# Kernel optimization log

Measured on AMD Instinct MI355X. Metric: run time of the kernel, lower is better.

The kernel has to match this reference:

```python
import jax, jax.numpy as jnp
import numpy as np

B, CIN, H, W = 32, 512, 16, 16
COUT, HEADS, SPARSITY = 2048, 8, 7
D = COUT // HEADS  # 256, must equal H*W
N = H * W


def conv1x1(x, w, b):
    # x: [B,C,H,W], w: [O,C], b: [O]
    return jnp.einsum('bchw,oc->bohw', x, w) + b[None, :, None, None]


def setup_inputs() -> dict:
    key = jax.random.key(0)
    ks = jax.random.split(key, 11)
    def lin(k, o, c):
        bound = 1.0 / np.sqrt(c)
        kw, kb = jax.random.split(k)
        return (jax.random.uniform(kw, (o, c), jnp.float32, -bound, bound),
                jax.random.uniform(kb, (o,), jnp.float32, -bound, bound))
    Wq, bq = lin(ks[0], COUT, CIN)
    Wk, bk = lin(ks[1], COUT, CIN)
    Wv, bv = lin(ks[2], COUT, CIN)
    Wo, bo = lin(ks[3], COUT, COUT)
    # kaiming_uniform_ on [COUT, COUT]
    gain = np.sqrt(2.0) / np.sqrt(5.0)  # default a=sqrt(5)
    bound = gain * np.sqrt(3.0 / COUT)
    coeff = jax.random.uniform(ks[4], (COUT, COUT), jnp.float32, -bound, bound)
    scale = jnp.array([np.sqrt(D)], jnp.float32)
    x = jax.random.normal(ks[5], (B, CIN, H, W), jnp.float32)
    return {"x": x, "Wq": Wq, "bq": bq, "Wk": Wk, "bk": bk, "Wv": Wv,
            "bv": bv, "Wo": Wo, "bo": bo, "coeff": coeff, "scale": scale}


def reference(x, Wq, bq, Wk, bk, Wv, bv, Wo, bo, coeff, scale):
    # enforce_sparsity: keep top-`SPARSITY` |coeff| per row, zero the rest
    _, idx = jax.lax.top_k(jnp.abs(coeff), SPARSITY)  # [COUT, SPARSITY]
    mask = jnp.zeros(coeff.shape, bool).at[jnp.arange(COUT)[:, None], idx].set(True)
    coeff_s = jnp.where(mask, coeff, 0.0)

    q = conv1x1(x, Wq, bq).reshape(B, HEADS, D, N)
    k = conv1x1(x, Wk, bk).reshape(B, HEADS, D, N)
    v = conv1x1(x, Wv, bv).reshape(B, HEADS, D, N)

    attn = jnp.einsum('bhdn,bhdm->bhnm', q, k) / scale[0]  # [B,h,N,N]
    sparse_attn = jnp.einsum('bhnm,mp->bhnp', attn, coeff_s[:D, :D])
    sparse_attn = jax.nn.softmax(sparse_attn, axis=-1)
    out = jnp.einsum('bhnm,bhmd->bhnd', sparse_attn, v.transpose(0, 1, 3, 2))
    out = out.transpose(0, 1, 3, 2).reshape(B, COUT, H, W)
    return conv1x1(out, Wo, bo)
```

## Files before the change

kernel.cpp:

```cpp
#include <hip/hip_runtime.h>

typedef unsigned short ushort;
typedef __attribute__((ext_vector_type(8))) short short8;
typedef __attribute__((ext_vector_type(8))) unsigned short ushort8;
typedef __attribute__((ext_vector_type(4))) unsigned short ushort4v;
typedef __attribute__((ext_vector_type(4))) float fx4;

#define MAXNNZ (256*7)

__device__ __forceinline__ ushort f2bf(float f) {
    union { float f; unsigned u; } v; v.f = f;
    unsigned r = v.u + 0x7fffu + ((v.u >> 16) & 1u);
    return (ushort)(r >> 16);
}

__device__ __forceinline__ float bf2f(ushort b) {
    union { unsigned u; float f; } v; v.u = ((unsigned)b) << 16;
    return v.f;
}

__device__ __forceinline__ void gload_lds16(const ushort* g, ushort* l) {
    __builtin_amdgcn_global_load_lds(
        (const __attribute__((address_space(1))) unsigned int*)g,
        (__attribute__((address_space(3))) unsigned int*)l, 16, 0, 0);
}

__global__ __launch_bounds__(256)
void topk_kernel(const float* __restrict__ coeff,
                 int* __restrict__ coo_cnt, int* __restrict__ coo_m,
                 int* __restrict__ coo_p, float* __restrict__ coo_v)
{
    int row = blockIdx.x;
    int tid = threadIdx.x;
    const float* crow = coeff + (long)row * 2048;
    float av[8];
#pragma unroll
    for (int i = 0; i < 8; ++i) av[i] = fabsf(crow[tid + 256 * i]);
    __shared__ unsigned long long red[256];
    for (int t = 0; t < 7; ++t) {
        float mx = -1.f; int mi = 0;
#pragma unroll
        for (int i = 0; i < 8; ++i) if (av[i] > mx) { mx = av[i]; mi = i; }
        unsigned col = (unsigned)(tid + 256 * mi);
        unsigned long long pk = ((unsigned long long)__float_as_uint(mx) << 32)
                              | (unsigned long long)(2048u - col);
        red[tid] = pk; __syncthreads();
        for (int s = 128; s > 0; s >>= 1) {
            if (tid < s) { if (red[tid + s] > red[tid]) red[tid] = red[tid + s]; }
            __syncthreads();
        }
        unsigned long long w = red[0];
        __syncthreads();
        unsigned wcol = 2048u - (unsigned)(w & 0xffffffffu);
        if ((wcol & 255u) == (unsigned)tid) av[wcol >> 8] = -1.f;
        if (tid == 0 && wcol < 256u) {
            int pos = atomicAdd(coo_cnt, 1);
            coo_m[pos] = row; coo_p[pos] = (int)wcol; coo_v[pos] = crow[wcol];
        }
    }
}

__global__ __launch_bounds__(256)
void csc_kernel(const int* __restrict__ coo_cnt, const int* __restrict__ coo_m,
                const int* __restrict__ coo_p, const float* __restrict__ coo_v,
                int* __restrict__ csc_ptr, int* __restrict__ csc_m, float* __restrict__ csc_v)
{
    __shared__ int cnt[256];
    __shared__ int off[257];
    __shared__ int cur[256];
    int tid = threadIdx.x;
    cnt[tid] = 0;
    __syncthreads();
    int n = *coo_cnt; if (n > MAXNNZ) n = MAXNNZ;
    for (int e = tid; e < n; e += 256) atomicAdd(&cnt[coo_p[e]], 1);
    __syncthreads();
    if (tid == 0) {
        int s = 0;
        for (int p = 0; p < 256; ++p) { off[p] = s; s += cnt[p]; }
        off[256] = s;
    }
    __syncthreads();
    csc_ptr[tid] = off[tid];
    if (tid == 0) csc_ptr[256] = off[256];
    cur[tid] = off[tid];
    __syncthreads();
    for (int e = tid; e < n; e += 256) {
        int p = coo_p[e];
        int pos = atomicAdd(&cur[p], 1);
        csc_m[pos] = coo_m[e];
        csc_v[pos] = coo_v[e];
    }
}

__global__ void cvt4_kernel(const float* a0, ushort* d0, int n0,
                            const float* a1, ushort* d1, int n1,
                            const float* a2, ushort* d2, int n2,
                            const float* a3, ushort* d3, int n3)
{
    const float* s; ushort* d; int n;
    switch (blockIdx.y) {
        case 0: s = a0; d = d0; n = n0; break;
        case 1: s = a1; d = d1; n = n1; break;
        case 2: s = a2; d = d2; n = n2; break;
        default: s = a3; d = d3; n = n3; break;
    }
    int nv = n >> 2;
    for (int i = blockIdx.x * blockDim.x + threadIdx.x; i < nv; i += gridDim.x * blockDim.x) {
        fx4 v = ((const fx4*)s)[i];
        ushort4v o;
        o[0] = f2bf(v[0]); o[1] = f2bf(v[1]); o[2] = f2bf(v[2]); o[3] = f2bf(v[3]);
        ((ushort4v*)d)[i] = o;
    }
}

__global__ __launch_bounds__(256)
void transpose_f32_bf16(const float* __restrict__ in, ushort* __restrict__ out, int R, int C)
{
    int z = blockIdx.z;
    const float* ib = in + (long)z * R * C;
    ushort* ob = out + (long)z * R * C;
    __shared__ ushort tile[64][72];
    int r0 = blockIdx.x * 64, c0 = blockIdx.y * 64;
    int tid = threadIdx.x;
    int rl = tid >> 2, sg = tid & 3;
#pragma unroll
    for (int h = 0; h < 4; ++h) {
        fx4 v = *(const fx4*)(ib + (long)(r0 + rl) * C + c0 + h * 16 + sg * 4);
#pragma unroll
        for (int i = 0; i < 4; ++i) tile[h * 16 + sg * 4 + i][rl] = f2bf(v[i]);
    }
    __syncthreads();
    int cl = rl;
#pragma unroll
    for (int h = 0; h < 2; ++h) {
        ushort8 vv = *(const ushort8*)(&tile[cl][h * 32 + sg * 8]);
        *(ushort8*)(ob + (long)(c0 + cl) * R + r0 + h * 32 + sg * 8) = vv;
    }
}

__global__ __launch_bounds__(256)
void kcomb_kernel(const ushort* __restrict__ kbT, ushort* __restrict__ ktc,
                  const int* __restrict__ csc_ptr, const int* __restrict__ csc_m,
                  const float* __restrict__ csc_v)
{
    int z = blockIdx.y;
    int tid = threadIdx.x;
    int p = blockIdx.x * 64 + (tid >> 2);
    int d0 = (tid & 3) * 64;
    const ushort* src = kbT + (long)z * 65536;
    float acc[64];
#pragma unroll
    for (int i = 0; i < 64; ++i) acc[i] = 0.f;
    int e0 = csc_ptr[p], e1 = csc_ptr[p + 1];
    for (int e = e0; e < e1; ++e) {
        const ushort* row = src + csc_m[e] * 256 + d0;
        float c = csc_v[e];
#pragma unroll
        for (int u = 0; u < 8; ++u) {
            ushort8 v = *(const ushort8*)(row + u * 8);
#pragma unroll
            for (int t = 0; t < 8; ++t) acc[u * 8 + t] += bf2f(v[t]) * c;
        }
    }
    ushort* dst = ktc + (long)z * 65536 + (long)p * 256 + d0;
#pragma unroll
    for (int u = 0; u < 8; ++u) {
        ushort8 o;
#pragma unroll
        for (int t = 0; t < 8; ++t) o[t] = f2bf(acc[u * 8 + t]);
        *(ushort8*)(dst + u * 8) = o;
    }
}

__global__ __launch_bounds__(512)
void attn_kernel(const ushort* __restrict__ Q, const ushort* __restrict__ Kt,
                 const ushort* __restrict__ V, ushort* __restrict__ O,
                 const float* __restrict__ scale_src)
{
    int z = blockIdx.x;
    int b = z >> 3, h = z & 7;
    const ushort* Qz = Q + (long)z * 65536;
    const ushort* Kz = Kt + (long)z * 65536;
    const ushort* Vz = V + (long)b * 524288 + (long)h * 65536;
    ushort* Ob = O + (long)b * 524288 + (long)h * 256;

    __shared__ __align__(16) ushort P[128 * 256];
    __shared__ __align__(16) ushort As[128 * 32];
    __shared__ __align__(16) ushort Bs[256 * 32];
    __shared__ __align__(16) ushort Vst[2][256 * 32];
    __shared__ float rmax[4][128];
    __shared__ float rsum[4][128];

    int tid = threadIdx.x;
    int wave = tid >> 6, lane = tid & 63;
    int l16 = lane & 15, quad = lane >> 4;

    int skey = (tid >> 3) & 3;
    int scol = ((tid & 3) ^ skey) * 8;
    int srow = tid >> 2;
    const ushort* qsrc  = Qz + (long)srow * 256 + scol;
    const ushort* ksrc0 = Kz + (long)srow * 256 + scol;
    const ushort* ksrc1 = ksrc0 + 128 * 256;
    const ushort* vsrc0 = Vz + (long)srow * 256 + scol;
    const ushort* vsrc1 = vsrc0 + 128 * 256;
    ushort* aDst  = As + wave * 512;
    ushort* bDst0 = Bs + wave * 512;
    ushort* bDst1 = Bs + 4096 + wave * 512;

    int rk = (l16 >> 1) & 3;
    float sc = 1.0f / scale_src[0];

    for (int hf = 0; hf < 2; ++hf) {
        int wrow = wave >> 2, wcol = wave & 3;
        fx4 acc[4][4];
#pragma unroll
        for (int i = 0; i < 4; ++i)
#pragma unroll
            for (int j = 0; j < 4; ++j) acc[i][j] = (fx4){0.f, 0.f, 0.f, 0.f};

        const ushort* qs = qsrc + (long)hf * 128 * 256;
        for (int kc = 0; kc < 256; kc += 32) {
            __syncthreads();
            gload_lds16(qs + kc, aDst);
            gload_lds16(ksrc0 + kc, bDst0);
            gload_lds16(ksrc1 + kc, bDst1);
            __syncthreads();
            short8 af[4], bf[4];
#pragma unroll
            for (int i = 0; i < 4; ++i)
                af[i] = *(const short8*)(As + (wrow * 64 + i * 16 + l16) * 32 + ((quad ^ rk) * 8));
#pragma unroll
            for (int j = 0; j < 4; ++j)
                bf[j] = *(const short8*)(Bs + (wcol * 64 + j * 16 + l16) * 32 + ((quad ^ rk) * 8));
#pragma unroll
            for (int i = 0; i < 4; ++i)
#pragma unroll
                for (int j = 0; j < 4; ++j)
                    acc[i][j] = __builtin_amdgcn_mfma_f32_16x16x32_bf16(af[i], bf[j], acc[i][j], 0, 0, 0);
        }

#pragma unroll
        for (int i = 0; i < 4; ++i)
#pragma unroll
            for (int j = 0; j < 4; ++j)
#pragma unroll
                for (int r = 0; r < 4; ++r) acc[i][j][r] *= sc;

        float lm[4][4];
#pragma unroll
        for (int i = 0; i < 4; ++i)
#pragma unroll
            for (int r = 0; r < 4; ++r) {
                float m = -1e30f;
#pragma unroll
                for (int j = 0; j < 4; ++j) m = fmaxf(m, acc[i][j][r]);
                lm[i][r] = m;
            }
#pragma unroll
        for (int d = 1; d < 16; d <<= 1)
#pragma unroll
            for (int i = 0; i < 4; ++i)
#pragma unroll
                for (int r = 0; r < 4; ++r) lm[i][r] = fmaxf(lm[i][r], __shfl_xor(lm[i][r], d, 16));
        if (l16 == 0) {
#pragma unroll
            for (int i = 0; i < 4; ++i)
#pragma unroll
                for (int r = 0; r < 4; ++r)
                    rmax[wcol][wrow * 64 + i * 16 + quad * 4 + r] = lm[i][r];
        }
        __syncthreads();

        float ls[4][4];
#pragma unroll
        for (int i = 0; i < 4; ++i)
#pragma unroll
            for (int r = 0; r < 4; ++r) {
                int row = wrow * 64 + i * 16 + quad * 4 + r;
                float M = fmaxf(fmaxf(rmax[0][row], rmax[1][row]),
                                fmaxf(rmax[2][row], rmax[3][row]));
                float s = 0.f;
#pragma unroll
                for (int j = 0; j < 4; ++j) {
                    float e = __expf(acc[i][j][r] - M);
                    acc[i][j][r] = e;
                    s += e;
                }
                ls[i][r] = s;
            }
#pragma unroll
        for (int d = 1; d < 16; d <<= 1)
#pragma unroll
            for (int i = 0; i < 4; ++i)
#pragma unroll
                for (int r = 0; r < 4; ++r) ls[i][r] += __shfl_xor(ls[i][r], d, 16);
        if (l16 == 0) {
#pragma unroll
            for (int i = 0; i < 4; ++i)
#pragma unroll
                for (int r = 0; r < 4; ++r)
                    rsum[wcol][wrow * 64 + i * 16 + quad * 4 + r] = ls[i][r];
        }
        __syncthreads();

#pragma unroll
        for (int i = 0; i < 4; ++i)
#pragma unroll
            for (int r = 0; r < 4; ++r) {
                int row = wrow * 64 + i * 16 + quad * 4 + r;
                float inv = 1.0f / (rsum[0][row] + rsum[1][row] + rsum[2][row] + rsum[3][row]);
                int key = row & 7;
#pragma unroll
                for (int j = 0; j < 4; ++j) {
                    int p = wcol * 64 + j * 16 + l16;
                    int idx = row * 256 + ((((p >> 3) ^ key) << 3) | (p & 7));
                    P[idx] = f2bf(acc[i][j][r] * inv);
                }
            }
        __syncthreads();

        int r2 = wave >> 2, c2 = wave & 3;
        fx4 acc2[4][4];
#pragma unroll
        for (int i = 0; i < 4; ++i)
#pragma unroll
            for (int j = 0; j < 4; ++j) acc2[i][j] = (fx4){0.f, 0.f, 0.f, 0.f};

        gload_lds16(vsrc0, Vst[0] + wave * 512);
        gload_lds16(vsrc1, Vst[0] + 4096 + wave * 512);
        __syncthreads();

        for (int kk = 0; kk < 8; ++kk) {
            short8 pa[4], vf[4];
#pragma unroll
            for (int i = 0; i < 4; ++i) {
                int row = r2 * 64 + i * 16 + l16;
                pa[i] = *(const short8*)(P + row * 256 + (((kk * 4 + quad) ^ (l16 & 7)) * 8));
            }
#pragma unroll
            for (int j = 0; j < 4; ++j)
                vf[j] = *(const short8*)(Vst[kk & 1] + (c2 * 64 + j * 16 + l16) * 32 + ((quad ^ rk) * 8));
            if (kk < 7) {
                gload_lds16(vsrc0 + (kk + 1) * 32, Vst[(kk + 1) & 1] + wave * 512);
                gload_lds16(vsrc1 + (kk + 1) * 32, Vst[(kk + 1) & 1] + 4096 + wave * 512);
            }
#pragma unroll
            for (int i = 0; i < 4; ++i)
#pragma unroll
                for (int j = 0; j < 4; ++j)
                    acc2[i][j] = __builtin_amdgcn_mfma_f32_16x16x32_bf16(pa[i], vf[j], acc2[i][j], 0, 0, 0);
            __syncthreads();
        }

#pragma unroll
        for (int i = 0; i < 4; ++i)
#pragma unroll
            for (int j = 0; j < 4; ++j) {
                int rowb = r2 * 64 + i * 16 + quad * 4;
                int col = c2 * 64 + j * 16 + l16;
#pragma unroll
                for (int rr = 0; rr < 4; ++rr) {
                    int row = rowb + rr;
                    int idx = row * 256 + ((((col >> 3) ^ (row & 7)) << 3) | (col & 7));
                    P[idx] = f2bf(acc2[i][j][rr]);
                }
            }
        __syncthreads();
#pragma unroll
        for (int pass = 0; pass < 8; ++pass) {
            int row = pass * 16 + (tid >> 5), ch = tid & 31;
            ushort8 v = *(const ushort8*)(P + row * 256 + ((ch ^ (row & 7)) << 3));
            *(ushort8*)(Ob + (long)(hf * 128 + row) * 2048 + ch * 8) = v;
        }
        __syncthreads();
    }
}

template<int MODE>
__global__ __launch_bounds__(512, 2)
void gemm256(const ushort* __restrict__ A, const ushort* __restrict__ B,
             void* __restrict__ C,
             const float* __restrict__ bias0, const float* __restrict__ bias1,
             const float* __restrict__ bias2,
             int MT, int K)
{
    __shared__ __align__(16) ushort lds[4][2][8192];

    int nwg = gridDim.x;
    int bid = blockIdx.x;
    int cpx = nwg >> 3;
    int swz = (bid & 7) * cpx + (bid >> 3);
    int mt = swz % MT, nt = swz / MT;
    int m0 = mt << 8, n0 = nt << 8;

    int tid = threadIdx.x;
    int wave = tid >> 6, lane = tid & 63;
    int wr = wave >> 2, wc = wave & 3;
    int l16 = lane & 15, quad = lane >> 4;

    int lc = (((lane & 3) ^ ((lane >> 3) & 3))) * 8;
    const ushort* gA0 = A + (long long)(m0 + wave * 16 + (lane >> 2)) * K + lc;
    const ushort* gA1 = gA0 + (long long)128 * K;
    const ushort* gB0 = B + (long long)(n0 + wave * 16 + (lane >> 2)) * K + lc;
    const ushort* gB1 = gB0 + (long long)128 * K;
    int ldso = wave * 512;

    int rsw = ((l16 >> 1) & 3) * 8;
    int aoff = (wr * 128 + l16) * 32 + ((quad * 8) ^ rsw);
    int boff = (wc * 64 + l16) * 32 + ((quad * 8) ^ rsw);

    fx4 acc[8][4];
#pragma unroll
    for (int i = 0; i < 8; ++i)
#pragma unroll
        for (int j = 0; j < 4; ++j) acc[i][j] = (fx4){0.f, 0.f, 0.f, 0.f};

    auto stageA = [&](int b, int kc) {
        gload_lds16(gA0 + kc, &lds[b][0][ldso]);
        gload_lds16(gA1 + kc, &lds[b][0][4096 + ldso]);
    };
    auto stageB = [&](int b, int kc) {
        gload_lds16(gB0 + kc, &lds[b][1][ldso]);
        gload_lds16(gB1 + kc, &lds[b][1][4096 + ldso]);
    };

    short8 af[4], bf[4];
    auto readA = [&](int b, int half) {
        const ushort* p = &lds[b][0][aoff + half * 2048];
#pragma unroll
        for (int i = 0; i < 4; ++i) af[i] = *(const short8*)(p + i * 512);
    };
    auto readB = [&](int b) {
        const ushort* p = &lds[b][1][boff];
#pragma unroll
        for (int j = 0; j < 4; ++j) bf[j] = *(const short8*)(p + j * 512);
    };
    auto mma = [&](int half) {
        __builtin_amdgcn_s_setprio(1);
#pragma unroll
        for (int i = 0; i < 4; ++i)
#pragma unroll
            for (int j = 0; j < 4; ++j)
                acc[half * 4 + i][j] =
                    __builtin_amdgcn_mfma_f32_16x16x32_bf16(af[i], bf[j], acc[half * 4 + i][j], 0, 0, 0);
        __builtin_amdgcn_s_setprio(0);
    };

    int NT = K >> 5;
    stageA(0, 0);  stageB(0, 0);
    stageA(1, 32); stageB(1, 32);
    stageA(2, 64); stageB(2, 64);
    asm volatile("s_waitcnt vmcnt(8)" ::: "memory");
    __builtin_amdgcn_s_barrier();

    for (int t = 0; t < NT; ++t) {
        int b = t & 3;
        readA(b, 0); readB(b);
        if (t + 3 < NT) stageA((t + 3) & 3, (t + 3) << 5);
        __builtin_amdgcn_s_barrier();
        asm volatile("s_waitcnt lgkmcnt(0)" ::: "memory");
        __builtin_amdgcn_sched_barrier(0);
        mma(0);
        __builtin_amdgcn_s_barrier();
        readA(b, 1);
        if (t + 3 < NT) {
            stageB((t + 3) & 3, (t + 3) << 5);
            asm volatile("s_waitcnt vmcnt(8)" ::: "memory");
        } else if (t + 2 < NT) {
            asm volatile("s_waitcnt vmcnt(4)" ::: "memory");
        } else if (t + 1 < NT) {
            asm volatile("s_waitcnt vmcnt(0)" ::: "memory");
        }
        __builtin_amdgcn_s_barrier();
        asm volatile("s_waitcnt lgkmcnt(0)" ::: "memory");
        __builtin_amdgcn_sched_barrier(0);
        mma(1);
        __builtin_amdgcn_s_barrier();
    }

    if (MODE == 5) {
        float* Cf = (float*)C + (long long)nt * 524288;
#pragma unroll
        for (int i = 0; i < 8; ++i) {
            int m = m0 + wr * 128 + i * 16 + quad * 4;
#pragma unroll
            for (int j = 0; j < 4; ++j) {
                int n = wc * 64 + j * 16 + l16;
                float* dst = Cf + (long long)m * 256 + n;
#pragma unroll
                for (int r = 0; r < 4; ++r)
                    dst[(long)r * 256] = acc[i][j][r] + bias0[m + r];
            }
        }
        return;
    }

    if (MODE == 4) {
        int sec = m0 >> 11;
        int ms0 = m0 & 2047;
        ushort* ct = &lds[0][0][0];
        if (sec < 2) {
            const float* bs = (sec == 0) ? bias0 : bias1;
            ushort* base = (ushort*)C + (long long)sec * 16777216
                         + (long long)nt * 524288 + (long long)(ms0 >> 8) * 65536;
#pragma unroll
            for (int hh = 0; hh < 2; ++hh) {
                if ((wc >> 1) == hh) {
#pragma unroll
                    for (int i = 0; i < 8; ++i)
#pragma unroll
                        for (int j = 0; j < 4; ++j) {
                            int nl = (wc & 1) * 64 + j * 16 + l16;
                            int ml = wr * 128 + i * 16 + quad * 4;
                            ushort4v pk;
#pragma unroll
                            for (int r = 0; r < 4; ++r)
                                pk[r] = f2bf(acc[i][j][r] + bs[ms0 + ml + r]);
                            *(ushort4v*)(ct + nl * 264 + ml) = pk;
                        }
                }
                __syncthreads();
                int row = tid & 127, c0 = (tid >> 7) * 64;
                ushort* dst = base + (long long)(hh * 128 + row) * 256 + c0;
                const ushort* src = ct + row * 264 + c0;
#pragma unroll
                for (int u = 0; u < 8; ++u)
                    *(ushort8*)(dst + u * 8) = *(const ushort8*)(src + u * 8);
                __syncthreads();
            }
        } else {
            ushort* base = (ushort*)C + 33554432LL + (long long)nt * 524288
                         + (long long)ms0 * 256;
#pragma unroll
            for (int hh = 0; hh < 2; ++hh) {
                if (wr == hh) {
#pragma unroll
                    for (int i = 0; i < 8; ++i)
#pragma unroll
                        for (int j = 0; j < 4; ++j) {
                            int nl = wc * 64 + j * 16 + l16;
                            int ml = i * 16 + quad * 4;
#pragma unroll
                            for (int r = 0; r < 4; ++r)
                                ct[(ml + r) * 264 + nl] =
                                    f2bf(acc[i][j][r] + bias2[ms0 + hh * 128 + ml + r]);
                        }
                }
                __syncthreads();
                int row = tid & 127, c0 = (tid >> 7) * 64;
                ushort* dst = base + (long long)(hh * 128 + row) * 256 + c0;
                const ushort* src = ct + row * 264 + c0;
#pragma unroll
                for (int u = 0; u < 8; ++u)
                    *(ushort8*)(dst + u * 8) = *(const ushort8*)(src + u * 8);
                __syncthreads();
            }
        }
        return;
    }
}

extern "C" void kernel_launch(void* const* d_in, const int* in_sizes, int n_in,
                              void* d_out, int out_size, void* d_ws, size_t ws_size,
                              hipStream_t stream)
{
    const float* x     = (const float*)d_in[0];
    const float* Wq    = (const float*)d_in[1];
    const float* bq    = (const float*)d_in[2];
    const float* Wk    = (const float*)d_in[3];
    const float* bk    = (const float*)d_in[4];
    const float* Wv    = (const float*)d_in[5];
    const float* bv    = (const float*)d_in[6];
    const float* Wo    = (const float*)d_in[7];
    const float* bo    = (const float*)d_in[8];
    const float* coeff = (const float*)d_in[9];
    const float* scale = (const float*)d_in[10];
    float* out = (float*)d_out;

    size_t o = 0;
    char* w = (char*)d_ws;
    auto take = [&](size_t bytes) -> void* {
        void* p = w + o; o += (bytes + 255) & ~(size_t)255; return p;
    };
    int*    coo_cnt = (int*)take(4);
    int*    coo_m   = (int*)take(MAXNNZ * 4);
    int*    coo_p   = (int*)take(MAXNNZ * 4);
    float*  coo_v   = (float*)take(MAXNNZ * 4);
    int*    csc_ptr = (int*)take(257 * 4);
    int*    csc_m   = (int*)take(MAXNNZ * 4);
    float*  csc_v   = (float*)take(MAXNNZ * 4);
    ushort* wqkv = (ushort*)take(6144L * 512 * 2);
    ushort* wob  = (ushort*)take(2048L * 2048 * 2);
    ushort* xT   = (ushort*)take(32L * 256 * 512 * 2);
    ushort* qkv  = (ushort*)take(3 * 16777216L * 2);
    ushort* qbT = qkv;
    ushort* kbT = qkv + 16777216L;
    ushort* vb  = qkv + 33554432L;
    ushort* ktc = (ushort*)take(16777216L * 2);
    ushort* obT  = kbT;
    (void)in_sizes; (void)n_in; (void)out_size; (void)ws_size;

    hipMemsetAsync(coo_cnt, 0, 4, stream);
    topk_kernel<<<256, 256, 0, stream>>>(coeff, coo_cnt, coo_m, coo_p, coo_v);
    csc_kernel<<<1, 256, 0, stream>>>(coo_cnt, coo_m, coo_p, coo_v, csc_ptr, csc_m, csc_v);

    cvt4_kernel<<<dim3(1024, 4, 1), 256, 0, stream>>>(
        Wq, wqkv, 2048 * 512, Wk, wqkv + 2048L * 512, 2048 * 512,
        Wv, wqkv + 4096L * 512, 2048 * 512, Wo, wob, 2048 * 2048);
    transpose_f32_bf16<<<dim3(8, 4, 32), 256, 0, stream>>>(x, xT, 512, 256);

    gemm256<4><<<dim3(768, 1, 1), dim3(512, 1, 1), 0, stream>>>(
        wqkv, xT, qkv, bq, bk, bv, 24, 512);

    kcomb_kernel<<<dim3(4, 256), 256, 0, stream>>>(kbT, ktc, csc_ptr, csc_m, csc_v);

    attn_kernel<<<256, 512, 0, stream>>>(qbT, ktc, vb, obT, scale);

    gemm256<5><<<dim3(256, 1, 1), dim3(512, 1, 1), 0, stream>>>(
        wob, obT, out, bo, nullptr, nullptr, 8, 2048);
}
```

Before: 401.5 us.

## Stage full Q tile in LDS and double-buffer 64-wide K/V chunks in attention

The attention kernel now loads the whole 128x256 Q half-tile into LDS once, reusing that buffer for P, and streams K and V in 64-column chunks through a double buffer. The next chunk's load is issued before the MFMAs on the current one, and V prefetch starts during softmax normalisation. Barriers become raw s_barrier with explicit waitcnt, plus setprio around the MFMA blocks. Together these aim to cut the barrier count and expose fewer global-load stalls, at the cost of more LDS, register pressure and fragile manual synchronisation.

```diff
diff --git a/kernel.cpp b/kernel.cpp
--- a/kernel.cpp
+++ b/kernel.cpp
@@ -177,6 +177,11 @@
                  const ushort* __restrict__ V, ushort* __restrict__ O,
                  const float* __restrict__ scale_src)
 {
+    __shared__ __align__(16) ushort PQ[32768];
+    __shared__ __align__(16) ushort KV[2][16384];
+    __shared__ float rmax[4][128];
+    __shared__ float rsum[4][128];
+
     int z = blockIdx.x;
     int b = z >> 3, h = z & 7;
     const ushort* Qz = Q + (long)z * 65536;
@@ -184,59 +189,67 @@
     const ushort* Vz = V + (long)b * 524288 + (long)h * 65536;
     ushort* Ob = O + (long)b * 524288 + (long)h * 256;
 
-    __shared__ __align__(16) ushort P[128 * 256];
-    __shared__ __align__(16) ushort As[128 * 32];
-    __shared__ __align__(16) ushort Bs[256 * 32];
-    __shared__ __align__(16) ushort Vst[2][256 * 32];
-    __shared__ float rmax[4][128];
-    __shared__ float rsum[4][128];
-
     int tid = threadIdx.x;
     int wave = tid >> 6, lane = tid & 63;
     int l16 = lane & 15, quad = lane >> 4;
-
-    int skey = (tid >> 3) & 3;
-    int scol = ((tid & 3) ^ skey) * 8;
-    int srow = tid >> 2;
-    const ushort* qsrc  = Qz + (long)srow * 256 + scol;
-    const ushort* ksrc0 = Kz + (long)srow * 256 + scol;
-    const ushort* ksrc1 = ksrc0 + 128 * 256;
-    const ushort* vsrc0 = Vz + (long)srow * 256 + scol;
-    const ushort* vsrc1 = vsrc0 + 128 * 256;
-    ushort* aDst  = As + wave * 512;
-    ushort* bDst0 = Bs + wave * 512;
-    ushort* bDst1 = Bs + 4096 + wave * 512;
-
-    int rk = (l16 >> 1) & 3;
+    int wrow = wave >> 2, wcol = wave & 3;
+    int key = l16 & 7;
+
+    const ushort* ksrc = Kz + (long)(tid >> 3) * 256 + (((tid & 7) ^ ((tid >> 3) & 7)) * 8);
+    const ushort* vsrc = Vz + (long)(tid >> 3) * 256 + (((tid & 7) ^ ((tid >> 3) & 7)) * 8);
+    const ushort* qsrc = Qz + (long)(tid >> 5) * 256 + (((tid & 31) ^ ((tid >> 5) & 7)) * 8);
+    int dstoff = wave * 512;
+
     float sc = 1.0f / scale_src[0];
 
     for (int hf = 0; hf < 2; ++hf) {
-        int wrow = wave >> 2, wcol = wave & 3;
+#pragma unroll
+        for (int g = 0; g < 8; ++g)
+            gload_lds16(qsrc + hf * 32768 + g * 4096, PQ + g * 4096 + dstoff);
+#pragma unroll
+        for (int g = 0; g < 4; ++g)
+            gload_lds16(ksrc + (long)g * 16384, KV[0] + g * 4096 + dstoff);
+
         fx4 acc[4][4];
 #pragma unroll
         for (int i = 0; i < 4; ++i)
 #pragma unroll
             for (int j = 0; j < 4; ++j) acc[i][j] = (fx4){0.f, 0.f, 0.f, 0.f};
 
-        const ushort* qs = qsrc + (long)hf * 128 * 256;
-        for (int kc = 0; kc < 256; kc += 32) {
-            __syncthreads();
-            gload_lds16(qs + kc, aDst);
-            gload_lds16(ksrc0 + kc, bDst0);
-            gload_lds16(ksrc1 + kc, bDst1);
-            __syncthreads();
-            short8 af[4], bf[4];
-#pragma unroll
-            for (int i = 0; i < 4; ++i)
-                af[i] = *(const short8*)(As + (wrow * 64 + i * 16 + l16) * 32 + ((quad ^ rk) * 8));
-#pragma unroll
-            for (int j = 0; j < 4; ++j)
-                bf[j] = *(const short8*)(Bs + (wcol * 64 + j * 16 + l16) * 32 + ((quad ^ rk) * 8));
-#pragma unroll
-            for (int i = 0; i < 4; ++i)
+        for (int t = 0; t < 4; ++t) {
+            asm volatile("s_waitcnt vmcnt(0)" ::: "memory");
+            __builtin_amdgcn_s_barrier();
+            if (t < 3) {
+#pragma unroll
+                for (int g = 0; g < 4; ++g)
+                    gload_lds16(ksrc + (long)g * 16384 + (t + 1) * 64,
+                                KV[(t + 1) & 1] + g * 4096 + dstoff);
+            }
+            const ushort* kb = KV[t & 1];
+            short8 af[8], bf[8];
+#pragma unroll
+            for (int ks = 0; ks < 2; ++ks) {
+#pragma unroll
+                for (int i = 0; i < 4; ++i)
+                    af[ks * 4 + i] = *(const short8*)(PQ + (wrow * 64 + i * 16 + l16) * 256
+                                     + ((((t * 2 + ks) * 4 + quad) ^ key) * 8));
 #pragma unroll
                 for (int j = 0; j < 4; ++j)
-                    acc[i][j] = __builtin_amdgcn_mfma_f32_16x16x32_bf16(af[i], bf[j], acc[i][j], 0, 0, 0);
+                    bf[ks * 4 + j] = *(const short8*)(kb + (wcol * 64 + j * 16 + l16) * 64
+                                     + (((ks * 4 + quad) ^ key) * 8));
+            }
+            asm volatile("s_waitcnt lgkmcnt(0)" ::: "memory");
+            __builtin_amdgcn_sched_barrier(0);
+            __builtin_amdgcn_s_setprio(1);
+#pragma unroll
+            for (int ks = 0; ks < 2; ++ks)
+#pragma unroll
+                for (int i = 0; i < 4; ++i)
+#pragma unroll
+                    for (int j = 0; j < 4; ++j)
+                        acc[i][j] = __builtin_amdgcn_mfma_f32_16x16x32_bf16(
+                            af[ks * 4 + i], bf[ks * 4 + j], acc[i][j], 0, 0, 0);
+            __builtin_amdgcn_s_setprio(0);
         }
 
 #pragma unroll
@@ -269,7 +282,8 @@
                 for (int r = 0; r < 4; ++r)
                     rmax[wcol][wrow * 64 + i * 16 + quad * 4 + r] = lm[i][r];
         }
-        __syncthreads();
+        asm volatile("s_waitcnt lgkmcnt(0)" ::: "memory");
+        __builtin_amdgcn_s_barrier();
 
         float ls[4][4];
 #pragma unroll
@@ -301,7 +315,12 @@
                 for (int r = 0; r < 4; ++r)
                     rsum[wcol][wrow * 64 + i * 16 + quad * 4 + r] = ls[i][r];
         }
-        __syncthreads();
+        asm volatile("s_waitcnt lgkmcnt(0)" ::: "memory");
+        __builtin_amdgcn_s_barrier();
+
+#pragma unroll
+        for (int g = 0; g < 4; ++g)
+            gload_lds16(vsrc + (long)g * 16384, KV[0] + g * 4096 + dstoff);
 
 #pragma unroll
         for (int i = 0; i < 4; ++i)
@@ -309,70 +328,81 @@
             for (int r = 0; r < 4; ++r) {
                 int row = wrow * 64 + i * 16 + quad * 4 + r;
                 float inv = 1.0f / (rsum[0][row] + rsum[1][row] + rsum[2][row] + rsum[3][row]);
-                int key = row & 7;
+                int k2 = row & 7;
 #pragma unroll
                 for (int j = 0; j < 4; ++j) {
                     int p = wcol * 64 + j * 16 + l16;
-                    int idx = row * 256 + ((((p >> 3) ^ key) << 3) | (p & 7));
-                    P[idx] = f2bf(acc[i][j][r] * inv);
+                    PQ[row * 256 + ((((p >> 3) ^ k2) << 3) | (p & 7))] = f2bf(acc[i][j][r] * inv);
                 }
             }
-        __syncthreads();
-
-        int r2 = wave >> 2, c2 = wave & 3;
+        asm volatile("s_waitcnt lgkmcnt(0)" ::: "memory");
+
         fx4 acc2[4][4];
 #pragma unroll
         for (int i = 0; i < 4; ++i)
 #pragma unroll
             for (int j = 0; j < 4; ++j) acc2[i][j] = (fx4){0.f, 0.f, 0.f, 0.f};
 
-        gload_lds16(vsrc0, Vst[0] + wave * 512);
-        gload_lds16(vsrc1, Vst[0] + 4096 + wave * 512);
-        __syncthreads();
-
-        for (int kk = 0; kk < 8; ++kk) {
-            short8 pa[4], vf[4];
-#pragma unroll
-            for (int i = 0; i < 4; ++i) {
-                int row = r2 * 64 + i * 16 + l16;
-                pa[i] = *(const short8*)(P + row * 256 + (((kk * 4 + quad) ^ (l16 & 7)) * 8));
-            }
-#pragma unroll
-            for (int j = 0; j < 4; ++j)
-                vf[j] = *(const short8*)(Vst[kk & 1] + (c2 * 64 + j * 16 + l16) * 32 + ((quad ^ rk) * 8));
-            if (kk < 7) {
-                gload_lds16(vsrc0 + (kk + 1) * 32, Vst[(kk + 1) & 1] + wave * 512);
-                gload_lds16(vsrc1 + (kk + 1) * 32, Vst[(kk + 1) & 1] + 4096 + wave * 512);
-            }
-#pragma unroll
-            for (int i = 0; i < 4; ++i)
+        for (int kk = 0; kk < 4; ++kk) {
+            asm volatile("s_waitcnt vmcnt(0)" ::: "memory");
+            __builtin_amdgcn_s_barrier();
+            if (kk < 3) {
+#pragma unroll
+                for (int g = 0; g < 4; ++g)
+                    gload_lds16(vsrc + (long)g * 16384 + (kk + 1) * 64,
+                                KV[(kk + 1) & 1] + g * 4096 + dstoff);
+            }
+            const ushort* vbuf = KV[kk & 1];
+            short8 pa[8], vf[8];
+#pragma unroll
+            for (int ks = 0; ks < 2; ++ks) {
+#pragma unroll
+                for (int i = 0; i < 4; ++i)
+                    pa[ks * 4 + i] = *(const short8*)(PQ + (wrow * 64 + i * 16 + l16) * 256
+                                     + ((((kk * 2 + ks) * 4 + quad) ^ key) * 8));
 #pragma unroll
                 for (int j = 0; j < 4; ++j)
-                    acc2[i][j] = __builtin_amdgcn_mfma_f32_16x16x32_bf16(pa[i], vf[j], acc2[i][j], 0, 0, 0);
-            __syncthreads();
-        }
-
+                    vf[ks * 4 + j] = *(const short8*)(vbuf + (wcol * 64 + j * 16 + l16) * 64
+                                     + (((ks * 4 + quad) ^ key) * 8));
+            }
+            asm volatile("s_waitcnt lgkmcnt(0)" ::: "memory");
+            __builtin_amdgcn_sched_barrier(0);
+            __builtin_amdgcn_s_setprio(1);
+#pragma unroll
+            for (int ks = 0; ks < 2; ++ks)
+#pragma unroll
+                for (int i = 0; i < 4; ++i)
+#pragma unroll
+                    for (int j = 0; j < 4; ++j)
+                        acc2[i][j] = __builtin_amdgcn_mfma_f32_16x16x32_bf16(
+                            pa[ks * 4 + i], vf[ks * 4 + j], acc2[i][j], 0, 0, 0);
+            __builtin_amdgcn_s_setprio(0);
+        }
+
+        __builtin_amdgcn_s_barrier();
 #pragma unroll
         for (int i = 0; i < 4; ++i)
 #pragma unroll
             for (int j = 0; j < 4; ++j) {
-                int rowb = r2 * 64 + i * 16 + quad * 4;
-                int col = c2 * 64 + j * 16 + l16;
+                int rowb = wrow * 64 + i * 16 + quad * 4;
+                int col = wcol * 64 + j * 16 + l16;
 #pragma unroll
                 for (int rr = 0; rr < 4; ++rr) {
                     int row = rowb + rr;
-                    int idx = row * 256 + ((((col >> 3) ^ (row & 7)) << 3) | (col & 7));
-                    P[idx] = f2bf(acc2[i][j][rr]);
+                    PQ[row * 256 + ((((col >> 3) ^ (row & 7)) << 3) | (col & 7))]
+                        = f2bf(acc2[i][j][rr]);
                 }
             }
-        __syncthreads();
+        asm volatile("s_waitcnt lgkmcnt(0)" ::: "memory");
+        __builtin_amdgcn_s_barrier();
 #pragma unroll
         for (int pass = 0; pass < 8; ++pass) {
             int row = pass * 16 + (tid >> 5), ch = tid & 31;
-            ushort8 v = *(const ushort8*)(P + row * 256 + ((ch ^ (row & 7)) << 3));
-            *(ushort8*)(Ob + (long)(hf * 128 + row) * 2048 + ch * 8) = v;
-        }
-        __syncthreads();
+            ushort8 vv = *(const ushort8*)(PQ + row * 256 + ((ch ^ (row & 7)) << 3));
+            *(ushort8*)(Ob + (long)(hf * 128 + row) * 2048 + ch * 8) = vv;
+        }
+        asm volatile("s_waitcnt lgkmcnt(0)" ::: "memory");
+        __builtin_amdgcn_s_barrier();
     }
 }
 
```

After: 420.5 us. 4.7% more time.

## Split attention per half into separate blocks with register-streamed K/V fragments

Applied to the files above, without the earlier changes.

The attention kernel now launches 512 blocks of 256 threads, one per (batch-head, query half), instead of 256 blocks that loop over both halves. The whole Q half-tile is loaded into LDS once, and each wave reads its K and V MFMA fragments straight from global memory into registers with one-step prefetch, removing the per-chunk LDS staging and barriers. MFMA sections are wrapped in s_setprio. This adds parallelism and removes synchronisation, at the cost of more accumulator registers per thread (8x4 tiles) and uncoalesced direct global fragment loads.

```diff
diff --git a/kernel.cpp b/kernel.cpp
--- a/kernel.cpp
+++ b/kernel.cpp
@@ -172,207 +172,209 @@
     }
 }
 
-__global__ __launch_bounds__(512)
+__global__ __launch_bounds__(256, 2)
 void attn_kernel(const ushort* __restrict__ Q, const ushort* __restrict__ Kt,
                  const ushort* __restrict__ V, ushort* __restrict__ O,
                  const float* __restrict__ scale_src)
 {
-    int z = blockIdx.x;
+    __shared__ __align__(16) ushort PQ[32768];
+    __shared__ float rmax[4][128];
+    __shared__ float rsum[4][128];
+
+    int bid = blockIdx.x;
+    int hf = bid >> 8, z = bid & 255;
     int b = z >> 3, h = z & 7;
-    const ushort* Qz = Q + (long)z * 65536;
+    const ushort* Qz = Q + (long)z * 65536 + (long)hf * 32768;
     const ushort* Kz = Kt + (long)z * 65536;
     const ushort* Vz = V + (long)b * 524288 + (long)h * 65536;
-    ushort* Ob = O + (long)b * 524288 + (long)h * 256;
-
-    __shared__ __align__(16) ushort P[128 * 256];
-    __shared__ __align__(16) ushort As[128 * 32];
-    __shared__ __align__(16) ushort Bs[256 * 32];
-    __shared__ __align__(16) ushort Vst[2][256 * 32];
-    __shared__ float rmax[4][128];
-    __shared__ float rsum[4][128];
+    ushort* Ob = O + (long)b * 524288 + (long)h * 256 + (long)hf * 128 * 2048;
 
     int tid = threadIdx.x;
     int wave = tid >> 6, lane = tid & 63;
     int l16 = lane & 15, quad = lane >> 4;
-
-    int skey = (tid >> 3) & 3;
-    int scol = ((tid & 3) ^ skey) * 8;
-    int srow = tid >> 2;
-    const ushort* qsrc  = Qz + (long)srow * 256 + scol;
-    const ushort* ksrc0 = Kz + (long)srow * 256 + scol;
-    const ushort* ksrc1 = ksrc0 + 128 * 256;
-    const ushort* vsrc0 = Vz + (long)srow * 256 + scol;
-    const ushort* vsrc1 = vsrc0 + 128 * 256;
-    ushort* aDst  = As + wave * 512;
-    ushort* bDst0 = Bs + wave * 512;
-    ushort* bDst1 = Bs + 4096 + wave * 512;
-
-    int rk = (l16 >> 1) & 3;
+    int key = l16 & 7;
+
+    {
+        int rb = wave * 2 + (lane >> 5);
+        const ushort* qsrc = Qz + (long)rb * 256 + (((lane & 31) ^ (rb & 7)) * 8);
+        ushort* qdst = PQ + wave * 512;
+#pragma unroll
+        for (int g = 0; g < 16; ++g)
+            gload_lds16(qsrc + g * 2048, qdst + g * 2048);
+    }
+
+    const ushort* kfp = Kz + (long)(wave * 64 + l16) * 256 + quad * 8;
+    const ushort* vfp = Vz + (long)(wave * 64 + l16) * 256 + quad * 8;
+
+    fx4 acc[8][4];
+#pragma unroll
+    for (int i = 0; i < 8; ++i)
+#pragma unroll
+        for (int j = 0; j < 4; ++j) acc[i][j] = (fx4){0.f, 0.f, 0.f, 0.f};
+
+    short8 bfn[4];
+#pragma unroll
+    for (int j = 0; j < 4; ++j) bfn[j] = *(const short8*)(kfp + j * 4096);
+
+    __syncthreads();
+
     float sc = 1.0f / scale_src[0];
 
-    for (int hf = 0; hf < 2; ++hf) {
-        int wrow = wave >> 2, wcol = wave & 3;
-        fx4 acc[4][4];
-#pragma unroll
-        for (int i = 0; i < 4; ++i)
-#pragma unroll
-            for (int j = 0; j < 4; ++j) acc[i][j] = (fx4){0.f, 0.f, 0.f, 0.f};
-
-        const ushort* qs = qsrc + (long)hf * 128 * 256;
-        for (int kc = 0; kc < 256; kc += 32) {
-            __syncthreads();
-            gload_lds16(qs + kc, aDst);
-            gload_lds16(ksrc0 + kc, bDst0);
-            gload_lds16(ksrc1 + kc, bDst1);
-            __syncthreads();
-            short8 af[4], bf[4];
-#pragma unroll
-            for (int i = 0; i < 4; ++i)
-                af[i] = *(const short8*)(As + (wrow * 64 + i * 16 + l16) * 32 + ((quad ^ rk) * 8));
+#pragma unroll
+    for (int kd = 0; kd < 8; ++kd) {
+        short8 bf[4];
+#pragma unroll
+        for (int j = 0; j < 4; ++j) bf[j] = bfn[j];
+        if (kd < 7) {
 #pragma unroll
             for (int j = 0; j < 4; ++j)
-                bf[j] = *(const short8*)(Bs + (wcol * 64 + j * 16 + l16) * 32 + ((quad ^ rk) * 8));
-#pragma unroll
-            for (int i = 0; i < 4; ++i)
-#pragma unroll
-                for (int j = 0; j < 4; ++j)
-                    acc[i][j] = __builtin_amdgcn_mfma_f32_16x16x32_bf16(af[i], bf[j], acc[i][j], 0, 0, 0);
-        }
-
-#pragma unroll
-        for (int i = 0; i < 4; ++i)
+                bfn[j] = *(const short8*)(kfp + j * 4096 + (kd + 1) * 32);
+        }
+        short8 af[8];
+#pragma unroll
+        for (int i = 0; i < 8; ++i)
+            af[i] = *(const short8*)(PQ + (i * 16 + l16) * 256 + (((kd * 4 + quad) ^ key) * 8));
+        __builtin_amdgcn_s_setprio(1);
+#pragma unroll
+        for (int i = 0; i < 8; ++i)
 #pragma unroll
             for (int j = 0; j < 4; ++j)
-#pragma unroll
-                for (int r = 0; r < 4; ++r) acc[i][j][r] *= sc;
-
-        float lm[4][4];
-#pragma unroll
-        for (int i = 0; i < 4; ++i)
-#pragma unroll
-            for (int r = 0; r < 4; ++r) {
-                float m = -1e30f;
-#pragma unroll
-                for (int j = 0; j < 4; ++j) m = fmaxf(m, acc[i][j][r]);
-                lm[i][r] = m;
+                acc[i][j] = __builtin_amdgcn_mfma_f32_16x16x32_bf16(af[i], bf[j], acc[i][j], 0, 0, 0);
+        __builtin_amdgcn_s_setprio(0);
+    }
+
+#pragma unroll
+    for (int i = 0; i < 8; ++i)
+#pragma unroll
+        for (int j = 0; j < 4; ++j)
+#pragma unroll
+            for (int r = 0; r < 4; ++r) acc[i][j][r] *= sc;
+
+    float lm[8][4];
+#pragma unroll
+    for (int i = 0; i < 8; ++i)
+#pragma unroll
+        for (int r = 0; r < 4; ++r) {
+            float m = -1e30f;
+#pragma unroll
+            for (int j = 0; j < 4; ++j) m = fmaxf(m, acc[i][j][r]);
+            lm[i][r] = m;
+        }
+#pragma unroll
+    for (int d = 1; d < 16; d <<= 1)
+#pragma unroll
+        for (int i = 0; i < 8; ++i)
+#pragma unroll
+            for (int r = 0; r < 4; ++r) lm[i][r] = fmaxf(lm[i][r], __shfl_xor(lm[i][r], d, 16));
+    if (l16 == 0) {
+#pragma unroll
+        for (int i = 0; i < 8; ++i)
+#pragma unroll
+            for (int r = 0; r < 4; ++r)
+                rmax[wave][i * 16 + quad * 4 + r] = lm[i][r];
+    }
+    __syncthreads();
+
+    float ls[8][4];
+#pragma unroll
+    for (int i = 0; i < 8; ++i)
+#pragma unroll
+        for (int r = 0; r < 4; ++r) {
+            int row = i * 16 + quad * 4 + r;
+            float M = fmaxf(fmaxf(rmax[0][row], rmax[1][row]),
+                            fmaxf(rmax[2][row], rmax[3][row]));
+            float s = 0.f;
+#pragma unroll
+            for (int j = 0; j < 4; ++j) {
+                float e = __expf(acc[i][j][r] - M);
+                acc[i][j][r] = e;
+                s += e;
             }
-#pragma unroll
-        for (int d = 1; d < 16; d <<= 1)
-#pragma unroll
-            for (int i = 0; i < 4; ++i)
-#pragma unroll
-                for (int r = 0; r < 4; ++r) lm[i][r] = fmaxf(lm[i][r], __shfl_xor(lm[i][r], d, 16));
-        if (l16 == 0) {
-#pragma unroll
-            for (int i = 0; i < 4; ++i)
-#pragma unroll
-                for (int r = 0; r < 4; ++r)
-                    rmax[wcol][wrow * 64 + i * 16 + quad * 4 + r] = lm[i][r];
-        }
-        __syncthreads();
-
-        float ls[4][4];
-#pragma unroll
-        for (int i = 0; i < 4; ++i)
-#pragma unroll
-            for (int r = 0; r < 4; ++r) {
-                int row = wrow * 64 + i * 16 + quad * 4 + r;
-                float M = fmaxf(fmaxf(rmax[0][row], rmax[1][row]),
-                                fmaxf(rmax[2][row], rmax[3][row]));
-                float s = 0.f;
-#pragma unroll
-                for (int j = 0; j < 4; ++j) {
-                    float e = __expf(acc[i][j][r] - M);
-                    acc[i][j][r] = e;
-                    s += e;
-                }
-                ls[i][r] = s;
+            ls[i][r] = s;
+        }
+#pragma unroll
+    for (int d = 1; d < 16; d <<= 1)
+#pragma unroll
+        for (int i = 0; i < 8; ++i)
+#pragma unroll
+            for (int r = 0; r < 4; ++r) ls[i][r] += __shfl_xor(ls[i][r], d, 16);
+    if (l16 == 0) {
+#pragma unroll
+        for (int i = 0; i < 8; ++i)
+#pragma unroll
+            for (int r = 0; r < 4; ++r)
+                rsum[wave][i * 16 + quad * 4 + r] = ls[i][r];
+    }
+    __syncthreads();
+
+    short8 vfn[4];
+#pragma unroll
+    for (int j = 0; j < 4; ++j) vfn[j] = *(const short8*)(vfp + j * 4096);
+
+#pragma unroll
+    for (int i = 0; i < 8; ++i)
+#pragma unroll
+        for (int r = 0; r < 4; ++r) {
+            int row = i * 16 + quad * 4 + r;
+            float inv = 1.0f / (rsum[0][row] + rsum[1][row] + rsum[2][row] + rsum[3][row]);
+            int k2 = row & 7;
+#pragma unroll
+            for (int j = 0; j < 4; ++j) {
+                int p = wave * 64 + j * 16 + l16;
+                PQ[row * 256 + ((((p >> 3) ^ k2) << 3) | (p & 7))] = f2bf(acc[i][j][r] * inv);
             }
-#pragma unroll
-        for (int d = 1; d < 16; d <<= 1)
-#pragma unroll
-            for (int i = 0; i < 4; ++i)
-#pragma unroll
-                for (int r = 0; r < 4; ++r) ls[i][r] += __shfl_xor(ls[i][r], d, 16);
-        if (l16 == 0) {
-#pragma unroll
-            for (int i = 0; i < 4; ++i)
-#pragma unroll
-                for (int r = 0; r < 4; ++r)
-                    rsum[wcol][wrow * 64 + i * 16 + quad * 4 + r] = ls[i][r];
-        }
-        __syncthreads();
-
-#pragma unroll
-        for (int i = 0; i < 4; ++i)
-#pragma unroll
-            for (int r = 0; r < 4; ++r) {
-                int row = wrow * 64 + i * 16 + quad * 4 + r;
-                float inv = 1.0f / (rsum[0][row] + rsum[1][row] + rsum[2][row] + rsum[3][row]);
-                int key = row & 7;
-#pragma unroll
-                for (int j = 0; j < 4; ++j) {
-                    int p = wcol * 64 + j * 16 + l16;
-                    int idx = row * 256 + ((((p >> 3) ^ key) << 3) | (p & 7));
-                    P[idx] = f2bf(acc[i][j][r] * inv);
-                }
+        }
+    __syncthreads();
+
+    fx4 acc2[8][4];
+#pragma unroll
+    for (int i = 0; i < 8; ++i)
+#pragma unroll
+        for (int j = 0; j < 4; ++j) acc2[i][j] = (fx4){0.f, 0.f, 0.f, 0.f};
+
+#pragma unroll
+    for (int kp = 0; kp < 8; ++kp) {
+        short8 vf[4];
+#pragma unroll
+        for (int j = 0; j < 4; ++j) vf[j] = vfn[j];
+        if (kp < 7) {
+#pragma unroll
+            for (int j = 0; j < 4; ++j)
+                vfn[j] = *(const short8*)(vfp + j * 4096 + (kp + 1) * 32);
+        }
+        short8 pa[8];
+#pragma unroll
+        for (int i = 0; i < 8; ++i)
+            pa[i] = *(const short8*)(PQ + (i * 16 + l16) * 256 + (((kp * 4 + quad) ^ key) * 8));
+        __builtin_amdgcn_s_setprio(1);
+#pragma unroll
+        for (int i = 0; i < 8; ++i)
+#pragma unroll
+            for (int j = 0; j < 4; ++j)
+                acc2[i][j] = __builtin_amdgcn_mfma_f32_16x16x32_bf16(pa[i], vf[j], acc2[i][j], 0, 0, 0);
+        __builtin_amdgcn_s_setprio(0);
+    }
+
+    __syncthreads();
+#pragma unroll
+    for (int i = 0; i < 8; ++i)
+#pragma unroll
+        for (int j = 0; j < 4; ++j) {
+            int rowb = i * 16 + quad * 4;
+            int col = wave * 64 + j * 16 + l16;
+#pragma unroll
+            for (int rr = 0; rr < 4; ++rr) {
+                int row = rowb + rr;
+                PQ[row * 256 + ((((col >> 3) ^ (row & 7)) << 3) | (col & 7))]
+                    = f2bf(acc2[i][j][rr]);
             }
-        __syncthreads();
-
-        int r2 = wave >> 2, c2 = wave & 3;
-        fx4 acc2[4][4];
-#pragma unroll
-        for (int i = 0; i < 4; ++i)
-#pragma unroll
-            for (int j = 0; j < 4; ++j) acc2[i][j] = (fx4){0.f, 0.f, 0.f, 0.f};
-
-        gload_lds16(vsrc0, Vst[0] + wave * 512);
-        gload_lds16(vsrc1, Vst[0] + 4096 + wave * 512);
-        __syncthreads();
-
-        for (int kk = 0; kk < 8; ++kk) {
-            short8 pa[4], vf[4];
-#pragma unroll
-            for (int i = 0; i < 4; ++i) {
-                int row = r2 * 64 + i * 16 + l16;
-                pa[i] = *(const short8*)(P + row * 256 + (((kk * 4 + quad) ^ (l16 & 7)) * 8));
-            }
-#pragma unroll
-            for (int j = 0; j < 4; ++j)
-                vf[j] = *(const short8*)(Vst[kk & 1] + (c2 * 64 + j * 16 + l16) * 32 + ((quad ^ rk) * 8));
-            if (kk < 7) {
-                gload_lds16(vsrc0 + (kk + 1) * 32, Vst[(kk + 1) & 1] + wave * 512);
-                gload_lds16(vsrc1 + (kk + 1) * 32, Vst[(kk + 1) & 1] + 4096 + wave * 512);
-            }
-#pragma unroll
-            for (int i = 0; i < 4; ++i)
-#pragma unroll
-                for (int j = 0; j < 4; ++j)
-                    acc2[i][j] = __builtin_amdgcn_mfma_f32_16x16x32_bf16(pa[i], vf[j], acc2[i][j], 0, 0, 0);
-            __syncthreads();
-        }
-
-#pragma unroll
-        for (int i = 0; i < 4; ++i)
-#pragma unroll
-            for (int j = 0; j < 4; ++j) {
-                int rowb = r2 * 64 + i * 16 + quad * 4;
-                int col = c2 * 64 + j * 16 + l16;
-#pragma unroll
-                for (int rr = 0; rr < 4; ++rr) {
-                    int row = rowb + rr;
-                    int idx = row * 256 + ((((col >> 3) ^ (row & 7)) << 3) | (col & 7));
-                    P[idx] = f2bf(acc2[i][j][rr]);
-                }
-            }
-        __syncthreads();
-#pragma unroll
-        for (int pass = 0; pass < 8; ++pass) {
-            int row = pass * 16 + (tid >> 5), ch = tid & 31;
-            ushort8 v = *(const ushort8*)(P + row * 256 + ((ch ^ (row & 7)) << 3));
-            *(ushort8*)(Ob + (long)(hf * 128 + row) * 2048 + ch * 8) = v;
-        }
-        __syncthreads();
+        }
+    __syncthreads();
+#pragma unroll
+    for (int pass = 0; pass < 16; ++pass) {
+        int row = pass * 8 + (tid >> 5), ch = tid & 31;
+        ushort8 vv = *(const ushort8*)(PQ + row * 256 + ((ch ^ (row & 7)) << 3));
+        *(ushort8*)(Ob + (long)row * 2048 + ch * 8) = vv;
     }
 }
 
@@ -614,7 +616,7 @@
 
     kcomb_kernel<<<dim3(4, 256), 256, 0, stream>>>(kbT, ktc, csc_ptr, csc_m, csc_v);
 
-    attn_kernel<<<256, 512, 0, stream>>>(qbT, ktc, vb, obT, scale);
+    attn_kernel<<<512, 256, 0, stream>>>(qbT, ktc, vb, obT, scale);
 
     gemm256<5><<<dim3(256, 1, 1), dim3(512, 1, 1), 0, stream>>>(
         wob, obT, out, bo, nullptr, nullptr, 8, 2048);
```

Result: faster. 381.1 us (-5.1%).
